# Kernel optimization log

Hardware: AMD Instinct MI355X
Metric: run time of the kernel (lower is better)

The kernel has to match this reference:

```python
import jax, jax.numpy as jnp
import numpy as np

NUM_NODES = 50000
NUM_EDGES = 800000
INPUT_DIM = 256
OUTPUT_DIM = 256
NUM_HEADS = 8
HEAD_DIM = OUTPUT_DIM // NUM_HEADS


def setup_inputs() -> dict:
    key = jax.random.key(0)
    ks = jax.random.split(key, 14)
    x = jax.random.normal(ks[0], (NUM_NODES, INPUT_DIM), dtype=jnp.float32)
    edge_index = jax.random.randint(ks[1], (2, NUM_EDGES), 0, NUM_NODES, dtype=jnp.int32)
    # timestamps in seconds over ~11.5 days so log1p(|dt|/3600) is informative
    edge_time = jax.random.uniform(ks[2], (NUM_EDGES,), dtype=jnp.float32) * 1e6
    node_time = jax.random.uniform(ks[3], (NUM_NODES,), dtype=jnp.float32) * 1e6
    s_in = 1.0 / np.sqrt(INPUT_DIM)
    s_out = 1.0 / np.sqrt(OUTPUT_DIM)
    s_t = 1.0 / np.sqrt(2.0)
    Wq = jax.random.uniform(ks[4], (INPUT_DIM, OUTPUT_DIM), jnp.float32, -s_in, s_in)
    bq = jax.random.uniform(ks[5], (OUTPUT_DIM,), jnp.float32, -s_in, s_in)
    Wk = jax.random.uniform(ks[6], (INPUT_DIM, OUTPUT_DIM), jnp.float32, -s_in, s_in)
    bk = jax.random.uniform(ks[7], (OUTPUT_DIM,), jnp.float32, -s_in, s_in)
    Wv = jax.random.uniform(ks[8], (INPUT_DIM, OUTPUT_DIM), jnp.float32, -s_in, s_in)
    bv = jax.random.uniform(ks[9], (OUTPUT_DIM,), jnp.float32, -s_in, s_in)
    Wt = jax.random.uniform(ks[10], (2, NUM_HEADS), jnp.float32, -s_t, s_t)
    bt = jax.random.uniform(ks[11], (NUM_HEADS,), jnp.float32, -s_t, s_t)
    Wo = jax.random.uniform(ks[12], (OUTPUT_DIM, OUTPUT_DIM), jnp.float32, -s_out, s_out)
    bo = jax.random.uniform(ks[13], (OUTPUT_DIM,), jnp.float32, -s_out, s_out)
    return {"x": x, "edge_index": edge_index, "edge_time": edge_time, "node_time": node_time,
            "Wq": Wq, "bq": bq, "Wk": Wk, "bk": bk, "Wv": Wv, "bv": bv,
            "Wt": Wt, "bt": bt, "Wo": Wo, "bo": bo}


def reference(x, edge_index, edge_time, node_time, Wq, bq, Wk, bk, Wv, bv, Wt, bt, Wo, bo):
    n = x.shape[0]
    q = (x @ Wq + bq).reshape(n, NUM_HEADS, HEAD_DIM)
    k = (x @ Wk + bk).reshape(n, NUM_HEADS, HEAD_DIM)
    v = (x @ Wv + bv).reshape(n, NUM_HEADS, HEAD_DIM)
    src, dst = edge_index[0], edge_index[1]
    # temporal features per edge
    time_diff = edge_time - node_time[dst]
    time_features = jnp.stack(
        [jnp.sign(time_diff), jnp.log1p(jnp.abs(time_diff) / 3600.0)], axis=-1)  # [E, 2]
    temporal_weights = time_features @ Wt + bt  # [E, H]
    scale = HEAD_DIM ** -0.5
    scores = jnp.einsum('ehd,ehd->eh', q[dst], k[src]) * scale + temporal_weights  # [E, H]
    # softmax over ALL edges per head (dim=0), as in the original
    alpha = jax.nn.softmax(scores, axis=0)  # [E, H]
    msg = alpha[..., None] * v[src]  # [E, H, D]
    out = jax.ops.segment_sum(msg, dst, num_segments=n)  # [N, H, D]
    out = out.reshape(n, OUTPUT_DIM)
    return out @ Wo + bo
```

## Files before the change

kernel.cpp:

```cpp
#include <hip/hip_runtime.h>
#include <hip/hip_bf16.h>

#define NUM_NODES 50000
#define NUM_EDGES 800000
#define NUM_HEADS 8
#define HEAD_DIM 32
#define SCAN_BLOCKS 49

typedef unsigned short ushort8 __attribute__((ext_vector_type(8)));
typedef float f32x4 __attribute__((ext_vector_type(4)));
typedef __bf16 bf16x8 __attribute__((ext_vector_type(8)));

union BF8 { ushort8 u; bf16x8 b; };

__device__ __forceinline__ unsigned float_to_key(float f) {
    int i = __float_as_int(f);
    return (i >= 0) ? ((unsigned)i | 0x80000000u) : ~(unsigned)i;
}
__device__ __forceinline__ float key_to_float(unsigned u) {
    unsigned b = (u & 0x80000000u) ? (u & 0x7fffffffu) : ~u;
    return __int_as_float((int)b);
}
__device__ __forceinline__ float bf2f(unsigned short u) {
    return __uint_as_float(((unsigned)u) << 16);
}
__device__ __forceinline__ unsigned short f2bf(float f) {
    unsigned u = __float_as_uint(f);
    unsigned r = (u + 0x7fffu + ((u >> 16) & 1u)) >> 16;
    return (unsigned short)r;
}

__global__ __launch_bounds__(256) void deg_kernel(const int* __restrict__ dst_idx, int* __restrict__ deg) {
    int e = blockIdx.x * 256 + threadIdx.x;
    if (e < NUM_EDGES) atomicAdd(&deg[dst_idx[e]], 1);
}

__global__ __launch_bounds__(1024) void scanA_kernel(
    const int* __restrict__ deg, int* __restrict__ offs, int* __restrict__ blocksum)
{
    __shared__ int buf[1024];
    int tid = threadIdx.x;
    int i = blockIdx.x * 1024 + tid;
    int v = (i < NUM_NODES) ? deg[i] : 0;
    buf[tid] = v;
    __syncthreads();
    for (int off = 1; off < 1024; off <<= 1) {
        int t = (tid >= off) ? buf[tid - off] : 0;
        __syncthreads();
        buf[tid] += t;
        __syncthreads();
    }
    if (i < NUM_NODES) offs[i] = buf[tid] - v;
    if (tid == 1023) blocksum[blockIdx.x] = buf[1023];
}

__global__ __launch_bounds__(64) void scanB_kernel(
    const int* __restrict__ blocksum, int* __restrict__ carry, int* __restrict__ offs)
{
    if (threadIdx.x == 0) {
        int acc = 0;
        for (int b = 0; b < SCAN_BLOCKS; b++) { carry[b] = acc; acc += blocksum[b]; }
        offs[NUM_NODES] = acc;
    }
}

__global__ __launch_bounds__(256) void scanC_kernel(
    int* __restrict__ offs, const int* __restrict__ carry, int* __restrict__ cursor)
{
    int i = blockIdx.x * 256 + threadIdx.x;
    if (i < NUM_NODES) {
        int v = offs[i] + carry[i >> 10];
        offs[i] = v;
        cursor[i] = v;
    }
}

__global__ __launch_bounds__(256) void fill2_kernel(
    const int* __restrict__ src_idx, const int* __restrict__ dst_idx,
    const float* __restrict__ edge_time, int* __restrict__ cursor,
    int* __restrict__ src_s, int* __restrict__ dst_s, float* __restrict__ et_s)
{
    int e = blockIdx.x * 256 + threadIdx.x;
    if (e < NUM_EDGES) {
        int d = dst_idx[e];
        int pos = atomicAdd(&cursor[d], 1);
        src_s[pos] = src_idx[e];
        dst_s[pos] = d;
        et_s[pos] = edge_time[e];
    }
}

__global__ __launch_bounds__(256) void wtrans_kernel(
    const float* __restrict__ Wq, const float* __restrict__ Wk,
    const float* __restrict__ Wv, const float* __restrict__ Wo,
    unsigned short* __restrict__ Wt)
{
    __shared__ float t[64][65];
    int nb = blockIdx.x * 64;
    int kb = blockIdx.y * 64;
    int g = nb >> 8;
    const float* W = (g == 0) ? Wq : (g == 1) ? Wk : (g == 2) ? Wv : Wo;
    int n0 = nb & 255;
    int tx = threadIdx.x & 63;
    int ty = threadIdx.x >> 6;
#pragma unroll
    for (int i = 0; i < 16; i++) {
        int k = i * 4 + ty;
        t[tx][k] = W[(size_t)(kb + k) * 256 + n0 + tx];
    }
    __syncthreads();
#pragma unroll
    for (int i = 0; i < 16; i++) {
        int n = i * 4 + ty;
        Wt[(size_t)(nb + n) * 256 + kb + tx] = f2bf(t[n][tx]);
    }
}

__global__ __launch_bounds__(256) void gemm_qkv_mfma3(
    const float* __restrict__ A, int M,
    const unsigned short* __restrict__ Wt,
    const float* __restrict__ b0, const float* __restrict__ b1, const float* __restrict__ b2,
    unsigned short* __restrict__ O0, unsigned short* __restrict__ O1, unsigned short* __restrict__ O2)
{
    __shared__ unsigned short As[64 * 256];
    int tid = threadIdx.x;
    int rowbase = blockIdx.x * 64;

    {
        int rsub = tid >> 6;
        int c4 = (tid & 63) * 4;
        int cchunk = (tid & 63) >> 1;
        int sub = (tid & 1);
#pragma unroll
        for (int it = 0; it < 16; it++) {
            int row = it * 4 + rsub;
            int grow = rowbase + row;
            float4 av = make_float4(0.f, 0.f, 0.f, 0.f);
            if (grow < M) av = *(const float4*)(A + (size_t)grow * 256 + c4);
            ushort4 o;
            o.x = f2bf(av.x); o.y = f2bf(av.y); o.z = f2bf(av.z); o.w = f2bf(av.w);
            unsigned byte = row * 512 + ((unsigned)(cchunk ^ (row & 7)) << 4) + sub * 8;
            *(ushort4*)((char*)As + byte) = o;
        }
    }
    __syncthreads();

    int lane = tid & 63;
    int wid = tid >> 6;
    int l16 = lane & 15;
    int kg = lane >> 4;

#pragma unroll
    for (int p = 0; p < 3; p++) {
        const float* bias = (p == 0) ? b0 : (p == 1) ? b1 : b2;
        unsigned short* O = (p == 0) ? O0 : (p == 1) ? O1 : O2;

        f32x4 acc[4][4];
#pragma unroll
        for (int m = 0; m < 4; m++)
#pragma unroll
            for (int n = 0; n < 4; n++) acc[m][n] = (f32x4)(0.0f);

        const unsigned short* wp[4];
#pragma unroll
        for (int n = 0; n < 4; n++)
            wp[n] = Wt + (size_t)(p * 256 + wid * 64 + n * 16 + l16) * 256 + kg * 8;

#pragma unroll
        for (int c2 = 0; c2 < 8; c2++) {
            bf16x8 wfr[4];
#pragma unroll
            for (int n = 0; n < 4; n++) {
                BF8 t; t.u = *(const ushort8*)(wp[n] + c2 * 32);
                wfr[n] = t.b;
            }
            bf16x8 afr[4];
#pragma unroll
            for (int m = 0; m < 4; m++) {
                int row = m * 16 + l16;
                int cchunk = (c2 * 4 + kg) ^ (row & 7);
                BF8 t;
                t.u = *(const ushort8*)((const char*)As + row * 512 + (cchunk << 4));
                afr[m] = t.b;
            }
#pragma unroll
            for (int m = 0; m < 4; m++)
#pragma unroll
                for (int n = 0; n < 4; n++)
                    acc[m][n] = __builtin_amdgcn_mfma_f32_16x16x32_bf16(wfr[n], afr[m], acc[m][n], 0, 0, 0);
        }

#pragma unroll
        for (int m = 0; m < 4; m++) {
            int node = rowbase + m * 16 + l16;
            if (node >= M) continue;
#pragma unroll
            for (int n = 0; n < 4; n++) {
                int lc = wid * 64 + n * 16 + kg * 4;
                float4 bv = *(const float4*)(bias + lc);
                ushort4 o;
                o.x = f2bf(acc[m][n][0] + bv.x);
                o.y = f2bf(acc[m][n][1] + bv.y);
                o.z = f2bf(acc[m][n][2] + bv.z);
                o.w = f2bf(acc[m][n][3] + bv.w);
                *(ushort4*)(O + (size_t)node * 256 + lc) = o;
            }
        }
    }
}

__global__ __launch_bounds__(256) void gemm_out_mfma3(
    const float* __restrict__ A, int M,
    const unsigned short* __restrict__ Wt,
    const float* __restrict__ bias, const float* __restrict__ kscale,
    float* __restrict__ C)
{
    __shared__ unsigned short As[64 * 256];
    int tid = threadIdx.x;
    int rowbase = blockIdx.x * 64;

    {
        int rsub = tid >> 6;
        int c4 = (tid & 63) * 4;
        int cchunk = (tid & 63) >> 1;
        int sub = (tid & 1);
        float ks = kscale[c4 >> 5];
#pragma unroll
        for (int it = 0; it < 16; it++) {
            int row = it * 4 + rsub;
            int grow = rowbase + row;
            float4 av = make_float4(0.f, 0.f, 0.f, 0.f);
            if (grow < M) av = *(const float4*)(A + (size_t)grow * 256 + c4);
            ushort4 o;
            o.x = f2bf(av.x * ks); o.y = f2bf(av.y * ks);
            o.z = f2bf(av.z * ks); o.w = f2bf(av.w * ks);
            unsigned byte = row * 512 + ((unsigned)(cchunk ^ (row & 7)) << 4) + sub * 8;
            *(ushort4*)((char*)As + byte) = o;
        }
    }
    __syncthreads();

    int lane = tid & 63;
    int wid = tid >> 6;
    int l16 = lane & 15;
    int kg = lane >> 4;

    f32x4 acc[4][4];
#pragma unroll
    for (int m = 0; m < 4; m++)
#pragma unroll
        for (int n = 0; n < 4; n++) acc[m][n] = (f32x4)(0.0f);

    const unsigned short* wp[4];
#pragma unroll
    for (int n = 0; n < 4; n++)
        wp[n] = Wt + (size_t)(wid * 64 + n * 16 + l16) * 256 + kg * 8;

#pragma unroll
    for (int c2 = 0; c2 < 8; c2++) {
        bf16x8 wfr[4];
#pragma unroll
        for (int n = 0; n < 4; n++) {
            BF8 t; t.u = *(const ushort8*)(wp[n] + c2 * 32);
            wfr[n] = t.b;
        }
        bf16x8 afr[4];
#pragma unroll
        for (int m = 0; m < 4; m++) {
            int row = m * 16 + l16;
            int cchunk = (c2 * 4 + kg) ^ (row & 7);
            BF8 t;
            t.u = *(const ushort8*)((const char*)As + row * 512 + (cchunk << 4));
            afr[m] = t.b;
        }
#pragma unroll
        for (int m = 0; m < 4; m++)
#pragma unroll
            for (int n = 0; n < 4; n++)
                acc[m][n] = __builtin_amdgcn_mfma_f32_16x16x32_bf16(wfr[n], afr[m], acc[m][n], 0, 0, 0);
    }

#pragma unroll
    for (int m = 0; m < 4; m++) {
        int node = rowbase + m * 16 + l16;
        if (node >= M) continue;
#pragma unroll
        for (int n = 0; n < 4; n++) {
            int col = wid * 64 + n * 16 + kg * 4;
            float4 bv = *(const float4*)(bias + col);
            float4 o;
            o.x = acc[m][n][0] + bv.x;
            o.y = acc[m][n][1] + bv.y;
            o.z = acc[m][n][2] + bv.z;
            o.w = acc[m][n][3] + bv.w;
            *(float4*)(C + (size_t)node * 256 + col) = o;
        }
    }
}

__global__ __launch_bounds__(256) void score2_kernel(
    const unsigned short* __restrict__ qb, const unsigned short* __restrict__ kb,
    const int* __restrict__ src_s, const int* __restrict__ dst_s,
    const float* __restrict__ et_s, const float* __restrict__ node_time,
    const float* __restrict__ Wt, const float* __restrict__ bt,
    float* __restrict__ scores, unsigned* __restrict__ partialmax)
{
    __shared__ unsigned smax[8];
    int tid = threadIdx.x;
    if (tid < 8) smax[tid] = 0u;
    __syncthreads();
    const int total = NUM_EDGES * 8;
    int t0 = blockIdx.x * 256 + tid;
    int stride = gridDim.x * 256;
    int h = t0 & 7;
    float wt0 = Wt[h], wt1 = Wt[8 + h], btv = bt[h];
    unsigned mykey = 0u;
    for (int t = t0; t < total; t += stride) {
        int pos = t >> 3;
        int s = src_s[pos], d = dst_s[pos];
        const ushort8* qp = (const ushort8*)(qb + (size_t)d * 256 + h * 32);
        const ushort8* kp = (const ushort8*)(kb + (size_t)s * 256 + h * 32);
        float dotv = 0.f;
#pragma unroll
        for (int i = 0; i < 4; i++) {
            ushort8 a = qp[i], b = kp[i];
#pragma unroll
            for (int j = 0; j < 8; j++) dotv += bf2f(a[j]) * bf2f(b[j]);
        }
        float td = et_s[pos] - node_time[d];
        float tf0 = (td > 0.f) ? 1.f : ((td < 0.f) ? -1.f : 0.f);
        float tf1 = log1pf(fabsf(td) * (1.f / 3600.f));
        float sc = dotv * 0.17677669529663687f + (tf0 * wt0 + tf1 * wt1 + btv);
        scores[t] = sc;
        unsigned kkey = float_to_key(sc);
        mykey = (kkey > mykey) ? kkey : mykey;
    }
    atomicMax(&smax[h], mykey);
    __syncthreads();
    if (tid < 8) partialmax[blockIdx.x * 8 + tid] = smax[tid];
}

__global__ __launch_bounds__(256) void reduce_max_kernel(
    const unsigned* __restrict__ partialmax, float* __restrict__ headmax)
{
    int tid = threadIdx.x;
    int h = tid >> 5, lane = tid & 31;
    unsigned m = 0u;
    for (int i = lane; i < 1024; i += 32) {
        unsigned v = partialmax[i * 8 + h];
        m = (v > m) ? v : m;
    }
    for (int off = 16; off > 0; off >>= 1) {
        unsigned o = __shfl_down(m, off, 32);
        m = (o > m) ? o : m;
    }
    if (lane == 0) headmax[h] = key_to_float(m);
}

__global__ __launch_bounds__(256) void aggregate3_kernel(
    const unsigned short* __restrict__ vb, const float* __restrict__ scores,
    const int* __restrict__ src_s, const int* __restrict__ offs,
    const float* __restrict__ headmax, float* __restrict__ agg,
    float* __restrict__ psum_part)
{
    __shared__ int ssrc[64];
    __shared__ float pl[64 * 8];
    __shared__ float hm[8];
    int n = blockIdx.x;
    int tid = threadIdx.x;
    int h = tid >> 5;
    if (tid < 8) hm[tid] = headmax[tid];
    __syncthreads();
    int start = offs[n], end = offs[n + 1];
    float acc = 0.f;
    float psum = 0.f;
    for (int cb = start; cb < end; cb += 64) {
        int cnt = min(64, end - cb);
        __syncthreads();
        if (tid < cnt) ssrc[tid] = src_s[cb + tid];
        {
            int i0 = tid;
            int j0 = i0 >> 3;
            if (j0 < cnt) pl[i0] = __expf(scores[(size_t)(cb + j0) * 8 + (i0 & 7)] - hm[i0 & 7]);
            int i1 = tid + 256;
            int j1 = i1 >> 3;
            if (j1 < cnt) pl[i1] = __expf(scores[(size_t)(cb + j1) * 8 + (i1 & 7)] - hm[i1 & 7]);
        }
        __syncthreads();
        for (int j = 0; j < cnt; j++) {
            int s = ssrc[j];
            float p = pl[j * 8 + h];
            acc += p * bf2f(vb[(size_t)s * 256 + tid]);
            psum += p;
        }
    }
    agg[(size_t)n * 256 + tid] = acc;
    if ((tid & 31) == 0) psum_part[(size_t)n * 8 + h] = psum;
}

__global__ __launch_bounds__(256) void reduce_sum_stage1(
    const float* __restrict__ psum_part, float* __restrict__ partial2)
{
    __shared__ float ssum[8];
    int tid = threadIdx.x;
    if (tid < 8) ssum[tid] = 0.f;
    __syncthreads();
    const int total = NUM_NODES * 8;
    int t0 = blockIdx.x * 256 + tid;
    int stride = gridDim.x * 256;
    int h = t0 & 7;
    float s = 0.f;
    for (int t = t0; t < total; t += stride) s += psum_part[t];
    atomicAdd(&ssum[h], s);
    __syncthreads();
    if (tid < 8) partial2[blockIdx.x * 8 + tid] = ssum[tid];
}

__global__ __launch_bounds__(256) void reduce_sum_final(
    const float* __restrict__ partial2, float* __restrict__ headinv)
{
    int tid = threadIdx.x;
    int h = tid >> 5, lane = tid & 31;
    float s = 0.f;
    for (int i = lane; i < 256; i += 32) s += partial2[i * 8 + h];
    for (int off = 16; off > 0; off >>= 1) s += __shfl_down(s, off, 32);
    if (lane == 0) headinv[h] = 1.f / s;
}

extern "C" void kernel_launch(void* const* d_in, const int* in_sizes, int n_in,
                              void* d_out, int out_size, void* d_ws, size_t ws_size,
                              hipStream_t stream) {
    const float* x = (const float*)d_in[0];
    const int* ei = (const int*)d_in[1];
    const int* src_idx = ei;
    const int* dst_idx = ei + NUM_EDGES;
    const float* edge_time = (const float*)d_in[2];
    const float* node_time = (const float*)d_in[3];
    const float* Wq = (const float*)d_in[4];  const float* bq = (const float*)d_in[5];
    const float* Wk = (const float*)d_in[6];  const float* bk = (const float*)d_in[7];
    const float* Wv = (const float*)d_in[8];  const float* bv = (const float*)d_in[9];
    const float* Wt = (const float*)d_in[10]; const float* bt = (const float*)d_in[11];
    const float* Wo = (const float*)d_in[12]; const float* bo = (const float*)d_in[13];
    float* out = (float*)d_out;

    char* w = (char*)d_ws;
    unsigned short* qb = (unsigned short*)w; w += (size_t)NUM_NODES * 256 * 2;
    unsigned short* kb = (unsigned short*)w; w += (size_t)NUM_NODES * 256 * 2;
    unsigned short* vb = (unsigned short*)w; w += (size_t)NUM_NODES * 256 * 2;
    float* scores = (float*)w;      w += (size_t)NUM_EDGES * 8 * 4;
    float* agg = (float*)w;         w += (size_t)NUM_NODES * 256 * 4;
    int* src_s = (int*)w;           w += (size_t)NUM_EDGES * 4;
    int* dst_s = (int*)w;           w += (size_t)NUM_EDGES * 4;
    float* et_s = (float*)w;        w += (size_t)NUM_EDGES * 4;
    int* deg = (int*)w;             w += (size_t)NUM_NODES * 4;
    int* offs = (int*)w;            w += (size_t)(NUM_NODES + 1) * 4;
    int* cursor = (int*)w;          w += (size_t)NUM_NODES * 4;
    unsigned* partialmax = (unsigned*)w; w += 1024 * 8 * 4;
    float* psum_part = (float*)w;   w += (size_t)NUM_NODES * 8 * 4;
    float* partial2 = (float*)w;    w += 256 * 8 * 4;
    float* headmax = (float*)w;     w += 8 * 4;
    float* headinv = (float*)w;     w += 8 * 4;
    int* blocksum = (int*)w;        w += 64 * 4;
    int* bcarry = (int*)w;          w += 64 * 4;
    unsigned short* Wtb = (unsigned short*)w; w += (size_t)1024 * 256 * 2;

    hipMemsetAsync(deg, 0, (size_t)NUM_NODES * 4, stream);

    dim3 gw(16, 4);
    wtrans_kernel<<<gw, 256, 0, stream>>>(Wq, Wk, Wv, Wo, Wtb);

    deg_kernel<<<(NUM_EDGES + 255) / 256, 256, 0, stream>>>(dst_idx, deg);
    scanA_kernel<<<SCAN_BLOCKS, 1024, 0, stream>>>(deg, offs, blocksum);
    scanB_kernel<<<1, 64, 0, stream>>>(blocksum, bcarry, offs);
    scanC_kernel<<<(NUM_NODES + 255) / 256, 256, 0, stream>>>(offs, bcarry, cursor);
    fill2_kernel<<<(NUM_EDGES + 255) / 256, 256, 0, stream>>>(src_idx, dst_idx, edge_time,
                                                              cursor, src_s, dst_s, et_s);

    gemm_qkv_mfma3<<<(NUM_NODES + 63) / 64, 256, 0, stream>>>(
        x, NUM_NODES, Wtb, bq, bk, bv, qb, kb, vb);

    score2_kernel<<<1024, 256, 0, stream>>>(qb, kb, src_s, dst_s, et_s, node_time,
                                            Wt, bt, scores, partialmax);
    reduce_max_kernel<<<1, 256, 0, stream>>>(partialmax, headmax);

    aggregate3_kernel<<<NUM_NODES, 256, 0, stream>>>(vb, scores, src_s, offs, headmax,
                                                     agg, psum_part);
    reduce_sum_stage1<<<256, 256, 0, stream>>>(psum_part, partial2);
    reduce_sum_final<<<1, 256, 0, stream>>>(partial2, headinv);

    gemm_out_mfma3<<<(NUM_NODES + 63) / 64, 256, 0, stream>>>(
        agg, NUM_NODES, Wtb + (size_t)768 * 256, bo, headinv, out);
}
```

Baseline: 414.2 us.

## Switch Q/K/V and scores to head-major layout and split aggregation by head

```diff
diff --git a/kernel.cpp b/kernel.cpp
--- a/kernel.cpp
+++ b/kernel.cpp
@@ -116,7 +116,7 @@
     }
 }
 
-__global__ __launch_bounds__(256) void gemm_qkv_mfma3(
+__global__ __launch_bounds__(256) void gemm_qkv_mfma4(
     const float* __restrict__ A, int M,
     const unsigned short* __restrict__ Wt,
     const float* __restrict__ b0, const float* __restrict__ b1, const float* __restrict__ b2,
@@ -203,14 +203,139 @@
                 o.y = f2bf(acc[m][n][1] + bv.y);
                 o.z = f2bf(acc[m][n][2] + bv.z);
                 o.w = f2bf(acc[m][n][3] + bv.w);
-                *(ushort4*)(O + (size_t)node * 256 + lc) = o;
+                int hh = lc >> 5, dd = lc & 31;
+                *(ushort4*)(O + ((size_t)hh * NUM_NODES + node) * 32 + dd) = o;
             }
         }
     }
 }
 
-__global__ __launch_bounds__(256) void gemm_out_mfma3(
-    const float* __restrict__ A, int M,
+__global__ __launch_bounds__(256) void score3_kernel(
+    const unsigned short* __restrict__ qh, const unsigned short* __restrict__ kh,
+    const int* __restrict__ src_s, const int* __restrict__ dst_s,
+    const float* __restrict__ et_s, const float* __restrict__ node_time,
+    const float* __restrict__ Wt, const float* __restrict__ bt,
+    float* __restrict__ scores, unsigned* __restrict__ partialmax)
+{
+    __shared__ unsigned sm;
+    int tid = threadIdx.x;
+    if (tid == 0) sm = 0u;
+    __syncthreads();
+    int h = blockIdx.x & 7;
+    int blk = blockIdx.x >> 3;
+    float wt0 = Wt[h], wt1 = Wt[8 + h], btv = bt[h];
+    const unsigned short* qhh = qh + (size_t)h * NUM_NODES * 32;
+    const unsigned short* khh = kh + (size_t)h * NUM_NODES * 32;
+    float* sc_h = scores + (size_t)h * NUM_EDGES;
+    unsigned mykey = 0u;
+    for (int pos = blk * 256 + tid; pos < NUM_EDGES; pos += 128 * 256) {
+        int s = src_s[pos], d = dst_s[pos];
+        const ushort8* qp = (const ushort8*)(qhh + (size_t)d * 32);
+        const ushort8* kp = (const ushort8*)(khh + (size_t)s * 32);
+        float dotv = 0.f;
+#pragma unroll
+        for (int i = 0; i < 4; i++) {
+            ushort8 a = qp[i], b = kp[i];
+#pragma unroll
+            for (int j = 0; j < 8; j++) dotv += bf2f(a[j]) * bf2f(b[j]);
+        }
+        float td = et_s[pos] - node_time[d];
+        float tf0 = (td > 0.f) ? 1.f : ((td < 0.f) ? -1.f : 0.f);
+        float tf1 = log1pf(fabsf(td) * (1.f / 3600.f));
+        float sc = dotv * 0.17677669529663687f + (tf0 * wt0 + tf1 * wt1 + btv);
+        sc_h[pos] = sc;
+        unsigned kkey = float_to_key(sc);
+        mykey = (kkey > mykey) ? kkey : mykey;
+    }
+#pragma unroll
+    for (int off = 32; off > 0; off >>= 1) {
+        unsigned o = __shfl_xor(mykey, off, 64);
+        mykey = (o > mykey) ? o : mykey;
+    }
+    if ((tid & 63) == 0) atomicMax(&sm, mykey);
+    __syncthreads();
+    if (tid == 0) partialmax[blockIdx.x] = sm;
+}
+
+__global__ __launch_bounds__(256) void reduce_max2_kernel(
+    const unsigned* __restrict__ partialmax, float* __restrict__ headmax)
+{
+    int tid = threadIdx.x;
+    int h = tid >> 5, lane = tid & 31;
+    unsigned m = 0u;
+#pragma unroll
+    for (int k = 0; k < 4; k++) {
+        unsigned v = partialmax[(lane + 32 * k) * 8 + h];
+        m = (v > m) ? v : m;
+    }
+    for (int off = 16; off > 0; off >>= 1) {
+        unsigned o = __shfl_down(m, off, 32);
+        m = (o > m) ? o : m;
+    }
+    if (lane == 0) headmax[h] = key_to_float(m);
+}
+
+__global__ __launch_bounds__(256) void aggregate4_kernel(
+    const unsigned short* __restrict__ vh, const float* __restrict__ scores,
+    const int* __restrict__ src_s, const int* __restrict__ offs,
+    const float* __restrict__ headmax, unsigned short* __restrict__ aggb,
+    float* __restrict__ psum_part)
+{
+    int tid = threadIdx.x;
+    int h = blockIdx.x & 7;
+    int ng = blockIdx.x >> 3;
+    int wave = tid >> 6;
+    int lane = tid & 63;
+    int node = ng * 4 + wave;
+    int j = lane >> 5, d = lane & 31;
+    float m = headmax[h];
+    const float* sc_h = scores + (size_t)h * NUM_EDGES;
+    const unsigned short* vhh = vh + (size_t)h * NUM_NODES * 32;
+    int start = offs[node], end = offs[node + 1];
+    float acc = 0.f, psum = 0.f;
+    for (int cb = start + j; cb < end; cb += 2) {
+        int s = src_s[cb];
+        float p = __expf(sc_h[cb] - m);
+        acc += p * bf2f(vhh[(size_t)s * 32 + d]);
+        psum += p;
+    }
+    acc += __shfl_down(acc, 32, 64);
+    psum += __shfl_down(psum, 32, 64);
+    if (lane < 32) aggb[((size_t)h * NUM_NODES + node) * 32 + d] = f2bf(acc);
+    if (lane == 0) psum_part[(size_t)node * 8 + h] = psum;
+}
+
+__global__ __launch_bounds__(256) void reduce_sum_stage1(
+    const float* __restrict__ psum_part, float* __restrict__ partial2)
+{
+    __shared__ float ssum[8];
+    int tid = threadIdx.x;
+    if (tid < 8) ssum[tid] = 0.f;
+    __syncthreads();
+    const int total = NUM_NODES * 8;
+    int t0 = blockIdx.x * 256 + tid;
+    int stride = gridDim.x * 256;
+    int h = t0 & 7;
+    float s = 0.f;
+    for (int t = t0; t < total; t += stride) s += psum_part[t];
+    atomicAdd(&ssum[h], s);
+    __syncthreads();
+    if (tid < 8) partial2[blockIdx.x * 8 + tid] = ssum[tid];
+}
+
+__global__ __launch_bounds__(256) void reduce_sum_final(
+    const float* __restrict__ partial2, float* __restrict__ headinv)
+{
+    int tid = threadIdx.x;
+    int h = tid >> 5, lane = tid & 31;
+    float s = 0.f;
+    for (int i = lane; i < 256; i += 32) s += partial2[i * 8 + h];
+    for (int off = 16; off > 0; off >>= 1) s += __shfl_down(s, off, 32);
+    if (lane == 0) headinv[h] = 1.f / s;
+}
+
+__global__ __launch_bounds__(256) void gemm_out_mfma4(
+    const unsigned short* __restrict__ aggb, int M,
     const unsigned short* __restrict__ Wt,
     const float* __restrict__ bias, const float* __restrict__ kscale,
     float* __restrict__ C)
@@ -224,16 +349,17 @@
         int c4 = (tid & 63) * 4;
         int cchunk = (tid & 63) >> 1;
         int sub = (tid & 1);
-        float ks = kscale[c4 >> 5];
+        int hh = c4 >> 5, dd = c4 & 31;
+        float ks = kscale[hh];
 #pragma unroll
         for (int it = 0; it < 16; it++) {
             int row = it * 4 + rsub;
             int grow = rowbase + row;
-            float4 av = make_float4(0.f, 0.f, 0.f, 0.f);
-            if (grow < M) av = *(const float4*)(A + (size_t)grow * 256 + c4);
+            ushort4 av = make_ushort4(0, 0, 0, 0);
+            if (grow < M) av = *(const ushort4*)(aggb + ((size_t)hh * NUM_NODES + grow) * 32 + dd);
             ushort4 o;
-            o.x = f2bf(av.x * ks); o.y = f2bf(av.y * ks);
-            o.z = f2bf(av.z * ks); o.w = f2bf(av.w * ks);
+            o.x = f2bf(bf2f(av.x) * ks); o.y = f2bf(bf2f(av.y) * ks);
+            o.z = f2bf(bf2f(av.z) * ks); o.w = f2bf(bf2f(av.w) * ks);
             unsigned byte = row * 512 + ((unsigned)(cchunk ^ (row & 7)) << 4) + sub * 8;
             *(ushort4*)((char*)As + byte) = o;
         }
@@ -296,135 +422,6 @@
             *(float4*)(C + (size_t)node * 256 + col) = o;
         }
     }
-}
-
-__global__ __launch_bounds__(256) void score2_kernel(
-    const unsigned short* __restrict__ qb, const unsigned short* __restrict__ kb,
-    const int* __restrict__ src_s, const int* __restrict__ dst_s,
-    const float* __restrict__ et_s, const float* __restrict__ node_time,
-    const float* __restrict__ Wt, const float* __restrict__ bt,
-    float* __restrict__ scores, unsigned* __restrict__ partialmax)
-{
-    __shared__ unsigned smax[8];
-    int tid = threadIdx.x;
-    if (tid < 8) smax[tid] = 0u;
-    __syncthreads();
-    const int total = NUM_EDGES * 8;
-    int t0 = blockIdx.x * 256 + tid;
-    int stride = gridDim.x * 256;
-    int h = t0 & 7;
-    float wt0 = Wt[h], wt1 = Wt[8 + h], btv = bt[h];
-    unsigned mykey = 0u;
-    for (int t = t0; t < total; t += stride) {
-        int pos = t >> 3;
-        int s = src_s[pos], d = dst_s[pos];
-        const ushort8* qp = (const ushort8*)(qb + (size_t)d * 256 + h * 32);
-        const ushort8* kp = (const ushort8*)(kb + (size_t)s * 256 + h * 32);
-        float dotv = 0.f;
-#pragma unroll
-        for (int i = 0; i < 4; i++) {
-            ushort8 a = qp[i], b = kp[i];
-#pragma unroll
-            for (int j = 0; j < 8; j++) dotv += bf2f(a[j]) * bf2f(b[j]);
-        }
-        float td = et_s[pos] - node_time[d];
-        float tf0 = (td > 0.f) ? 1.f : ((td < 0.f) ? -1.f : 0.f);
-        float tf1 = log1pf(fabsf(td) * (1.f / 3600.f));
-        float sc = dotv * 0.17677669529663687f + (tf0 * wt0 + tf1 * wt1 + btv);
-        scores[t] = sc;
-        unsigned kkey = float_to_key(sc);
-        mykey = (kkey > mykey) ? kkey : mykey;
-    }
-    atomicMax(&smax[h], mykey);
-    __syncthreads();
-    if (tid < 8) partialmax[blockIdx.x * 8 + tid] = smax[tid];
-}
-
-__global__ __launch_bounds__(256) void reduce_max_kernel(
-    const unsigned* __restrict__ partialmax, float* __restrict__ headmax)
-{
-    int tid = threadIdx.x;
-    int h = tid >> 5, lane = tid & 31;
-    unsigned m = 0u;
-    for (int i = lane; i < 1024; i += 32) {
-        unsigned v = partialmax[i * 8 + h];
-        m = (v > m) ? v : m;
-    }
-    for (int off = 16; off > 0; off >>= 1) {
-        unsigned o = __shfl_down(m, off, 32);
-        m = (o > m) ? o : m;
-    }
-    if (lane == 0) headmax[h] = key_to_float(m);
-}
-
-__global__ __launch_bounds__(256) void aggregate3_kernel(
-    const unsigned short* __restrict__ vb, const float* __restrict__ scores,
-    const int* __restrict__ src_s, const int* __restrict__ offs,
-    const float* __restrict__ headmax, float* __restrict__ agg,
-    float* __restrict__ psum_part)
-{
-    __shared__ int ssrc[64];
-    __shared__ float pl[64 * 8];
-    __shared__ float hm[8];
-    int n = blockIdx.x;
-    int tid = threadIdx.x;
-    int h = tid >> 5;
-    if (tid < 8) hm[tid] = headmax[tid];
-    __syncthreads();
-    int start = offs[n], end = offs[n + 1];
-    float acc = 0.f;
-    float psum = 0.f;
-    for (int cb = start; cb < end; cb += 64) {
-        int cnt = min(64, end - cb);
-        __syncthreads();
-        if (tid < cnt) ssrc[tid] = src_s[cb + tid];
-        {
-            int i0 = tid;
-            int j0 = i0 >> 3;
-            if (j0 < cnt) pl[i0] = __expf(scores[(size_t)(cb + j0) * 8 + (i0 & 7)] - hm[i0 & 7]);
-            int i1 = tid + 256;
-            int j1 = i1 >> 3;
-            if (j1 < cnt) pl[i1] = __expf(scores[(size_t)(cb + j1) * 8 + (i1 & 7)] - hm[i1 & 7]);
-        }
-        __syncthreads();
-        for (int j = 0; j < cnt; j++) {
-            int s = ssrc[j];
-            float p = pl[j * 8 + h];
-            acc += p * bf2f(vb[(size_t)s * 256 + tid]);
-            psum += p;
-        }
-    }
-    agg[(size_t)n * 256 + tid] = acc;
-    if ((tid & 31) == 0) psum_part[(size_t)n * 8 + h] = psum;
-}
-
-__global__ __launch_bounds__(256) void reduce_sum_stage1(
-    const float* __restrict__ psum_part, float* __restrict__ partial2)
-{
-    __shared__ float ssum[8];
-    int tid = threadIdx.x;
-    if (tid < 8) ssum[tid] = 0.f;
-    __syncthreads();
-    const int total = NUM_NODES * 8;
-    int t0 = blockIdx.x * 256 + tid;
-    int stride = gridDim.x * 256;
-    int h = t0 & 7;
-    float s = 0.f;
-    for (int t = t0; t < total; t += stride) s += psum_part[t];
-    atomicAdd(&ssum[h], s);
-    __syncthreads();
-    if (tid < 8) partial2[blockIdx.x * 8 + tid] = ssum[tid];
-}
-
-__global__ __launch_bounds__(256) void reduce_sum_final(
-    const float* __restrict__ partial2, float* __restrict__ headinv)
-{
-    int tid = threadIdx.x;
-    int h = tid >> 5, lane = tid & 31;
-    float s = 0.f;
-    for (int i = lane; i < 256; i += 32) s += partial2[i * 8 + h];
-    for (int off = 16; off > 0; off >>= 1) s += __shfl_down(s, off, 32);
-    if (lane == 0) headinv[h] = 1.f / s;
 }
 
 extern "C" void kernel_launch(void* const* d_in, const int* in_sizes, int n_in,
@@ -448,14 +445,14 @@
     unsigned short* kb = (unsigned short*)w; w += (size_t)NUM_NODES * 256 * 2;
     unsigned short* vb = (unsigned short*)w; w += (size_t)NUM_NODES * 256 * 2;
     float* scores = (float*)w;      w += (size_t)NUM_EDGES * 8 * 4;
-    float* agg = (float*)w;         w += (size_t)NUM_NODES * 256 * 4;
+    unsigned short* aggb = (unsigned short*)w; w += (size_t)NUM_NODES * 256 * 2;
     int* src_s = (int*)w;           w += (size_t)NUM_EDGES * 4;
     int* dst_s = (int*)w;           w += (size_t)NUM_EDGES * 4;
     float* et_s = (float*)w;        w += (size_t)NUM_EDGES * 4;
     int* deg = (int*)w;             w += (size_t)NUM_NODES * 4;
     int* offs = (int*)w;            w += (size_t)(NUM_NODES + 1) * 4;
     int* cursor = (int*)w;          w += (size_t)NUM_NODES * 4;
-    unsigned* partialmax = (unsigned*)w; w += 1024 * 8 * 4;
+    unsigned* partialmax = (unsigned*)w; w += 1024 * 4;
     float* psum_part = (float*)w;   w += (size_t)NUM_NODES * 8 * 4;
     float* partial2 = (float*)w;    w += 256 * 8 * 4;
     float* headmax = (float*)w;     w += 8 * 4;
@@ -476,18 +473,18 @@
     fill2_kernel<<<(NUM_EDGES + 255) / 256, 256, 0, stream>>>(src_idx, dst_idx, edge_time,
                                                               cursor, src_s, dst_s, et_s);
 
-    gemm_qkv_mfma3<<<(NUM_NODES + 63) / 64, 256, 0, stream>>>(
+    gemm_qkv_mfma4<<<(NUM_NODES + 63) / 64, 256, 0, stream>>>(
         x, NUM_NODES, Wtb, bq, bk, bv, qb, kb, vb);
 
-    score2_kernel<<<1024, 256, 0, stream>>>(qb, kb, src_s, dst_s, et_s, node_time,
+    score3_kernel<<<1024, 256, 0, stream>>>(qb, kb, src_s, dst_s, et_s, node_time,
                                             Wt, bt, scores, partialmax);
-    reduce_max_kernel<<<1, 256, 0, stream>>>(partialmax, headmax);
-
-    aggregate3_kernel<<<NUM_NODES, 256, 0, stream>>>(vb, scores, src_s, offs, headmax,
-                                                     agg, psum_part);
+    reduce_max2_kernel<<<1, 256, 0, stream>>>(partialmax, headmax);
+
+    aggregate4_kernel<<<(NUM_NODES / 4) * 8, 256, 0, stream>>>(
+        vb, scores, src_s, offs, headmax, aggb, psum_part);
     reduce_sum_stage1<<<256, 256, 0, stream>>>(psum_part, partial2);
     reduce_sum_final<<<1, 256, 0, stream>>>(partial2, headinv);
 
-    gemm_out_mfma3<<<(NUM_NODES + 63) / 64, 256, 0, stream>>>(
-        agg, NUM_NODES, Wtb + (size_t)768 * 256, bo, headinv, out);
-}
+    gemm_out_mfma4<<<(NUM_NODES + 63) / 64, 256, 0, stream>>>(
+        aggb, NUM_NODES, Wtb + (size_t)768 * 256, bo, headinv, out);
+}
```

After: 531.0 us. 1.28x slower.
